# Kernel tuning notes

Hardware: AMD Instinct MI355X
Metric: run time of the kernel (lower is better)

Reference implementation:

```python
import jax, jax.numpy as jnp
from jax import lax
import numpy as np

B, T, LAT, HID, OUT, NC = 1024, 128, 128, 256, 128, 2
HODE = 128          # ODEFunc hidden width (hard-coded 128 in source)
H = LAT // 2        # LSTM hidden = latent_dim / 2


def setup_inputs() -> dict:
    key = jax.random.key(0)
    ks = jax.random.split(key, 8)
    s = 0.05
    f32 = jnp.float32
    return {
        "initial_state": jax.random.normal(ks[0], (B, LAT), f32),
        "time_steps": jnp.linspace(0.0, 1.0, T, dtype=f32),
        "ode_w1": jax.random.normal(ks[1], (HODE, LAT), f32) * s,
        "ode_b1": jnp.zeros((HODE,), f32),
        "ode_w2": jax.random.normal(ks[2], (LAT, HODE), f32) * s,
        "ode_b2": jnp.zeros((LAT,), f32),
        "l2h_w": jax.random.normal(ks[3], (HID, LAT), f32) * s,
        "l2h_b": jnp.zeros((HID,), f32),
        "h2o_w": jax.random.normal(ks[4], (OUT, HID), f32) * s,
        "h2o_b": jnp.zeros((OUT,), f32),
        "lstm_wih": jax.random.normal(ks[5], (4 * H, LAT), f32) * s,
        "lstm_whh": jax.random.normal(ks[6], (4 * H, H), f32) * s,
        "lstm_bih": jnp.zeros((4 * H,), f32),
        "lstm_bhh": jnp.zeros((4 * H,), f32),
        "fc2_w": jax.random.normal(ks[7], (NC, H), f32) * s,
        "fc2_b": jnp.zeros((NC,), f32),
    }


def reference(initial_state, time_steps, ode_w1, ode_b1, ode_w2, ode_b2,
              l2h_w, l2h_b, h2o_w, h2o_b,
              lstm_wih, lstm_whh, lstm_bih, lstm_bhh, fc2_w, fc2_b):
    def ode_f(y):  # Linear-ELU-Linear, time-independent
        return jax.nn.elu(y @ ode_w1.T + ode_b1) @ ode_w2.T + ode_b2

    def rk4_step(y, dt):
        k1 = ode_f(y)
        k2 = ode_f(y + 0.5 * dt * k1)
        k3 = ode_f(y + 0.5 * dt * k2)
        k4 = ode_f(y + dt * k3)
        y_new = y + (dt / 6.0) * (k1 + 2.0 * k2 + 2.0 * k3 + k4)
        return y_new, y_new

    dts = time_steps[1:] - time_steps[:-1]
    _, ys = lax.scan(rk4_step, initial_state, dts)
    zs = jnp.concatenate([initial_state[None], ys], axis=0)  # [T, B, LAT] = odeint output

    # torch: cat((initial_state.unsqueeze(0), zs)).permute(1,0,2) -> [B, T+1, LAT]
    input_lstm = jnp.concatenate([initial_state[None], zs], axis=0).transpose(1, 0, 2)

    # nn.LSTM is seq-first, so it scans dim0 (=B) with dim1 (=T+1) as its batch.
    h0 = jnp.zeros((input_lstm.shape[1], H), input_lstm.dtype)
    c0 = jnp.zeros_like(h0)

    def cell(carry, x):
        h, c = carry
        gates = x @ lstm_wih.T + lstm_bih + h @ lstm_whh.T + lstm_bhh
        i, f, g, o = jnp.split(gates, 4, axis=-1)  # torch gate order i,f,g,o
        c = jax.nn.sigmoid(f) * c + jax.nn.sigmoid(i) * jnp.tanh(g)
        h = jax.nn.sigmoid(o) * jnp.tanh(c)
        return (h, c), h

    _, lstm_hs = lax.scan(cell, (h0, c0), input_lstm)  # [B, T+1, H]
    lstm_out = lstm_hs[:, -1, :] @ fc2_w.T + fc2_b      # [B, NC]

    hs = zs @ l2h_w.T + l2h_b   # [T, B, HID]
    xs = hs @ h2o_w.T + h2o_b   # [T, B, OUT]
    return xs, lstm_out
```

## Files before the change

### kernel.cpp

```cpp
#include <hip/hip_runtime.h>


typedef short s16x8 __attribute__((ext_vector_type(8)));
typedef float f32x4 __attribute__((ext_vector_type(4)));
typedef _Float16 f16x2 __attribute__((ext_vector_type(2)));
typedef _Float16 f16x8 __attribute__((ext_vector_type(8)));

#define MFMA16(a, b, c) __builtin_amdgcn_mfma_f32_16x16x32_bf16((a), (b), (c), 0, 0, 0)

__device__ __forceinline__ void lds_barrier() {
  asm volatile("s_waitcnt lgkmcnt(0)\n\ts_barrier" ::: "memory");
}

__device__ __forceinline__ unsigned short f2bf(float x) {
  union { float f; unsigned u; } v; v.f = x;
  return (unsigned short)((v.u + 0x7FFFu + ((v.u >> 16) & 1u)) >> 16);
}

__device__ __forceinline__ unsigned cvtpk(float lo, float hi) {
  unsigned r;
  asm("v_cvt_pk_bf16_f32 %0, %1, %2" : "=v"(r) : "v"(lo), "v"(hi));
  return r;
}

__device__ __forceinline__ int swz(int row, int col2) {
  return row * 256 + (col2 ^ ((row & 15) << 4));
}

__device__ __forceinline__ f16x8 cvt8(const float* p) {
  float4 a = *(const float4*)p, b = *(const float4*)(p + 4);
  return (f16x8){(_Float16)a.x, (_Float16)a.y, (_Float16)a.z, (_Float16)a.w,
                 (_Float16)b.x, (_Float16)b.y, (_Float16)b.z, (_Float16)b.w};
}

__global__ __launch_bounds__(256, 1) void ode_kernel(
    const float* __restrict__ init, const float* __restrict__ ts,
    const float* __restrict__ w1, const float* __restrict__ b1,
    const float* __restrict__ w2, const float* __restrict__ b2,
    const float* __restrict__ wih, const float* __restrict__ bih,
    const float* __restrict__ bhh,
    unsigned short* __restrict__ zbuf, float* __restrict__ XW4)
{
  __shared__ __align__(16) unsigned char sY[4096];
  __shared__ __align__(16) unsigned char sH[4096];
  __shared__ __align__(16) float sYf[2048];
  const int tid = (int)threadIdx.x;
  const int w = tid >> 6, lane = tid & 63;
  const int l15 = lane & 15, l4 = lane >> 4;
  const int rowbase = (int)blockIdx.x * 16;
  const int colbase = w * 32;

  s16x8 w1f[2][4], w2f[2][4];
#pragma unroll
  for (int tc = 0; tc < 2; ++tc) {
    const int rj = colbase + 16 * tc + l15;
#pragma unroll
    for (int ks = 0; ks < 4; ++ks) {
      const int kb = ks * 32 + l4 * 8;
      s16x8 va, vb;
#pragma unroll
      for (int t = 0; t < 8; ++t) {
        va[t] = (short)f2bf(w1[rj * 128 + kb + t]);
        vb[t] = (short)f2bf(w2[rj * 128 + kb + t]);
      }
      w1f[tc][ks] = va; w2f[tc][ks] = vb;
    }
  }
  float b1v[2], b2v[2];
#pragma unroll
  for (int tc = 0; tc < 2; ++tc) {
    const int cc = colbase + 16 * tc + l15;
    b1v[tc] = b1[cc]; b2v[tc] = b2[cc];
  }

  int aOff[4];
#pragma unroll
  for (int ks = 0; ks < 4; ++ks) aOff[ks] = swz(l15, (ks * 32 + l4 * 8) * 2);
  int cOff[2][4];
#pragma unroll
  for (int tc = 0; tc < 2; ++tc)
#pragma unroll
    for (int r = 0; r < 4; ++r)
      cOff[tc][r] = swz(l4 * 4 + r, (colbase + 16 * tc + l15) * 2);

  float y0[2][4], yac[2][4];
#pragma unroll
  for (int tc = 0; tc < 2; ++tc)
#pragma unroll
    for (int r = 0; r < 4; ++r)
      y0[tc][r] = init[(rowbase + l4 * 4 + r) * 128 + colbase + 16 * tc + l15];

  {
    const int i = tid * 8;
    const int row = i >> 7, col = i & 127;
    union { unsigned short u[8]; s16x8 v; } p;
#pragma unroll
    for (int t = 0; t < 8; ++t) p.u[t] = f2bf(init[(rowbase + row) * 128 + col + t]);
    *(s16x8*)(sY + swz(row, col * 2)) = p.v;
    *(s16x8*)(zbuf + rowbase * 128 + i) = p.v;
  }
  __syncthreads();

  const f32x4 fz = {0.f, 0.f, 0.f, 0.f};

  for (int s = 0; s < 127; ++s) {
    const float dt = ts[s + 1] - ts[s];
    const float c16 = dt * (1.f / 6.f), c13 = dt * (1.f / 3.f), ch = dt * 0.5f;
#pragma unroll
    for (int st = 0; st < 4; ++st) {
      f32x4 acc[2];
      acc[0] = fz; acc[1] = fz;
#pragma unroll
      for (int ks = 0; ks < 4; ++ks) {
        s16x8 a = *(const s16x8*)(sY + aOff[ks]);
        acc[0] = MFMA16(a, w1f[0][ks], acc[0]);
        acc[1] = MFMA16(a, w1f[1][ks], acc[1]);
      }
#pragma unroll
      for (int r = 0; r < 4; ++r) {
        float v0 = acc[0][r] + b1v[0];
        float v1 = acc[1][r] + b1v[1];
        v0 = v0 > 0.f ? v0 : (__expf(v0) - 1.f);
        v1 = v1 > 0.f ? v1 : (__expf(v1) - 1.f);
        const unsigned p = cvtpk(v0, v1);
        *(unsigned short*)(sH + cOff[0][r]) = (unsigned short)p;
        *(unsigned short*)(sH + cOff[1][r]) = (unsigned short)(p >> 16);
      }
      lds_barrier();
      f32x4 kc[2];
      kc[0] = fz; kc[1] = fz;
#pragma unroll
      for (int ks = 0; ks < 4; ++ks) {
        s16x8 a = *(const s16x8*)(sH + aOff[ks]);
        kc[0] = MFMA16(a, w2f[0][ks], kc[0]);
        kc[1] = MFMA16(a, w2f[1][ks], kc[1]);
      }
#pragma unroll
      for (int r = 0; r < 4; ++r) {
        float yn2[2];
#pragma unroll
        for (int tc = 0; tc < 2; ++tc) {
          const float kv = kc[tc][r] + b2v[tc];
          float yn;
          if (st == 0)      { yac[tc][r] = fmaf(c16, kv, y0[tc][r]);  yn = fmaf(ch, kv, y0[tc][r]); }
          else if (st == 1) { yac[tc][r] = fmaf(c13, kv, yac[tc][r]); yn = fmaf(ch, kv, y0[tc][r]); }
          else if (st == 2) { yac[tc][r] = fmaf(c13, kv, yac[tc][r]); yn = fmaf(dt, kv, y0[tc][r]); }
          else              { y0[tc][r]  = fmaf(c16, kv, yac[tc][r]); yn = y0[tc][r]; }
          yn2[tc] = yn;
        }
        const unsigned p = cvtpk(yn2[0], yn2[1]);
        *(unsigned short*)(sY + cOff[0][r]) = (unsigned short)p;
        *(unsigned short*)(sY + cOff[1][r]) = (unsigned short)(p >> 16);
      }
      lds_barrier();
    }
    {
      const int i = tid * 8;
      const int row = i >> 7;
      const s16x8 v = *(const s16x8*)(sY + swz(row, (i & 127) * 2));
      *(s16x8*)(zbuf + (long)(s + 1) * 131072 + rowbase * 128 + i) = v;
    }
  }
#pragma unroll
  for (int tc = 0; tc < 2; ++tc)
#pragma unroll
    for (int r = 0; r < 4; ++r)
      sYf[(l4 * 4 + r) * 128 + colbase + 16 * tc + l15] = y0[tc][r];
  lds_barrier();
  {
    const int g = tid;
    const int q = g >> 6, j = g & 63;
#pragma unroll 4
    for (int tl = 0; tl < 16; ++tl) {
      float a0 = 0.f, a1 = 0.f, a2 = 0.f, a3 = 0.f;
#pragma unroll 8
      for (int k = 0; k < 32; ++k) {
        float4 wv = *(const float4*)(wih + g * 128 + 4 * k);
        float4 yv = *(const float4*)(sYf + tl * 128 + 4 * k);
        a0 = fmaf(wv.x, yv.x, a0); a1 = fmaf(wv.y, yv.y, a1);
        a2 = fmaf(wv.z, yv.z, a2); a3 = fmaf(wv.w, yv.w, a3);
      }
      XW4[(rowbase + tl) * 256 + j * 4 + q] = bih[g] + bhh[g] + ((a0 + a1) + (a2 + a3));
    }
  }
}

__global__ __launch_bounds__(128) void wf_kernel(
    const float* __restrict__ h2o, const float* __restrict__ l2h,
    const float* __restrict__ l2hb, const float* __restrict__ h2ob,
    unsigned short* __restrict__ wfo, float* __restrict__ bfo)
{
  const int o = (int)blockIdx.x, k = (int)threadIdx.x;
  float acc = 0.f;
  for (int h = 0; h < 256; ++h) acc = fmaf(h2o[o * 256 + h], l2h[h * 128 + k], acc);
  wfo[o * 128 + k] = f2bf(acc);
  __shared__ float red[128];
  red[k] = h2o[o * 256 + k] * l2hb[k] + h2o[o * 256 + 128 + k] * l2hb[128 + k];
  __syncthreads();
  for (int s = 64; s > 0; s >>= 1) {
    if (k < s) red[k] += red[k + s];
    __syncthreads();
  }
  if (k == 0) bfo[o] = red[0] + h2ob[o];
}

__device__ __forceinline__ void proj_body(
    const unsigned short* __restrict__ zbuf, const unsigned short* __restrict__ wf,
    const float* __restrict__ bfv_, float* __restrict__ xs)
{
  const int tid = (int)threadIdx.x;
  const int w = tid >> 6, lane = tid & 63;
  const int l15 = lane & 15, l4 = lane >> 4;
  const int colbase = w * 32;
  const long rowbase = (long)(blockIdx.x - 1) * 64;

  s16x8 wff[2][4];
#pragma unroll
  for (int tc = 0; tc < 2; ++tc) {
    const int rj = colbase + 16 * tc + l15;
#pragma unroll
    for (int ks = 0; ks < 4; ++ks)
      wff[tc][ks] = *(const s16x8*)(wf + rj * 128 + ks * 32 + l4 * 8);
  }
  const float bv0 = bfv_[colbase + l15], bv1 = bfv_[colbase + 16 + l15];

  const f32x4 fz = {0.f, 0.f, 0.f, 0.f};
  f32x4 acc[4][2];
#pragma unroll
  for (int rt = 0; rt < 4; ++rt) { acc[rt][0] = fz; acc[rt][1] = fz; }

#pragma unroll
  for (int rt = 0; rt < 4; ++rt) {
    const long rb = rowbase + rt * 16 + l15;
#pragma unroll
    for (int ks = 0; ks < 4; ++ks) {
      const s16x8 a = *(const s16x8*)(zbuf + rb * 128 + ks * 32 + l4 * 8);
      acc[rt][0] = MFMA16(a, wff[0][ks], acc[rt][0]);
      acc[rt][1] = MFMA16(a, wff[1][ks], acc[rt][1]);
    }
  }
#pragma unroll
  for (int rt = 0; rt < 4; ++rt)
#pragma unroll
    for (int r = 0; r < 4; ++r) {
      const long row = rowbase + rt * 16 + l4 * 4 + r;
      xs[row * 128 + colbase + l15]      = acc[rt][0][r] + bv0;
      xs[row * 128 + colbase + 16 + l15] = acc[rt][1][r] + bv1;
    }
}

__device__ __forceinline__ void lstm_body(
    const float* __restrict__ XW4,
    const float* __restrict__ whh,
    float* __restrict__ hsT)
{
  const int tid = (int)threadIdx.x;
  const int L = tid & 63;
  const int q = L & 3;
  const int j = (tid >> 6) * 16 + (L >> 2);
  const int row = q * 64 + j;

  __shared__ __align__(16) _Float16 hbuf[2][64];

  f16x8 wq[8];
#pragma unroll
  for (int k = 0; k < 8; ++k) wq[k] = cvt8(whh + row * 64 + 8 * k);

  const float Aa = (q == 2) ? 2.f : 1.f;
  const float Sa = (q == 2) ? -2.f : -1.f;
  const float Ba = (q == 2) ? -1.f : 0.f;

  if (tid < 64) hbuf[0][tid] = (_Float16)0.f;
  float c = 0.f;

  const int xwi = j * 4 + q;
  float xq[4];
#pragma unroll
  for (int i = 0; i < 4; ++i) xq[i] = XW4[i * 256 + xwi];
  lds_barrier();

  for (int tb = 0; tb < 256; ++tb) {
#pragma unroll
    for (int i = 0; i < 4; ++i) {
      const int t = tb * 4 + i;
      const int cur = i & 1;
      const float xw = xq[i];
      xq[i] = XW4[((t + 4) & 1023) * 256 + xwi];

      const f16x8* hb8 = (const f16x8*)hbuf[cur];
      float4 ac0 = {0.f, 0.f, 0.f, 0.f}, ac1 = {0.f, 0.f, 0.f, 0.f};
#pragma unroll
      for (int r = 0; r < 8; ++r) {
        const f16x8 v = hb8[r];
        float4& ac = (r & 1) ? ac1 : ac0;
        ac.x = __builtin_amdgcn_fdot2(__builtin_shufflevector(wq[r], wq[r], 0, 1),
                                      __builtin_shufflevector(v, v, 0, 1), ac.x, false);
        ac.y = __builtin_amdgcn_fdot2(__builtin_shufflevector(wq[r], wq[r], 2, 3),
                                      __builtin_shufflevector(v, v, 2, 3), ac.y, false);
        ac.z = __builtin_amdgcn_fdot2(__builtin_shufflevector(wq[r], wq[r], 4, 5),
                                      __builtin_shufflevector(v, v, 4, 5), ac.z, false);
        ac.w = __builtin_amdgcn_fdot2(__builtin_shufflevector(wq[r], wq[r], 6, 7),
                                      __builtin_shufflevector(v, v, 6, 7), ac.w, false);
      }
      const float pre = xw + (((ac0.x + ac0.y) + (ac0.z + ac0.w)) +
                              ((ac1.x + ac1.y) + (ac1.z + ac1.w)));
      const float act = fmaf(Aa, __builtin_amdgcn_rcpf(1.f + __expf(Sa * pre)), Ba);

      const int ai = __float_as_int(act);
      const float x1 = __int_as_float(__builtin_amdgcn_mov_dpp(ai, 0xB1, 0xF, 0xF, true));
      const float x2 = __int_as_float(__builtin_amdgcn_mov_dpp(ai, 0x4E, 0xF, 0xF, true));
      const float x3 = __int_as_float(__builtin_amdgcn_mov_dpp(ai, 0x1B, 0xF, 0xF, true));
      const float gi = (q == 0) ? act : (q == 1) ? x1 : (q == 2) ? x2 : x3;
      const float gf = (q == 0) ? x1 : (q == 1) ? act : (q == 2) ? x3 : x2;
      const float gg = (q == 0) ? x2 : (q == 1) ? x3 : (q == 2) ? act : x1;
      const float go = (q == 0) ? x3 : (q == 1) ? x2 : (q == 2) ? x1 : act;

      c = fmaf(gf, c, gi * gg);
      const float th = fmaf(2.f, __builtin_amdgcn_rcpf(1.f + __expf(-2.f * c)), -1.f);
      const float h = go * th;

      if (q == 0) {
        hbuf[cur ^ 1][j] = (_Float16)h;
        hsT[j * 1024 + t] = h;
      }
      lds_barrier();
    }
  }
}

__global__ __launch_bounds__(256, 1) void proj_lstm_kernel(
    const unsigned short* __restrict__ zbuf, const unsigned short* __restrict__ wf,
    const float* __restrict__ bfv_, float* __restrict__ xs,
    const float* __restrict__ XW4, const float* __restrict__ whh,
    float* __restrict__ hsT)
{
  if (blockIdx.x == 0) lstm_body(XW4, whh, hsT);
  else                 proj_body(zbuf, wf, bfv_, xs);
}

__global__ __launch_bounds__(256) void fc2_kernel(
    const float* __restrict__ hsT, const float* __restrict__ fw,
    const float* __restrict__ fb, float* __restrict__ lout)
{
  const int idx = (int)blockIdx.x * 256 + (int)threadIdx.x;
  const int n = idx >> 10, t = idx & 1023;
  float acc = fb[n];
#pragma unroll 8
  for (int j = 0; j < 64; ++j) acc = fmaf(fw[n * 64 + j], hsT[j * 1024 + t], acc);
  lout[t * 2 + n] = acc;
}

extern "C" void kernel_launch(void* const* d_in, const int* in_sizes, int n_in,
                              void* d_out, int out_size, void* d_ws, size_t ws_size,
                              hipStream_t stream) {
  const float* init  = (const float*)d_in[0];
  const float* ts    = (const float*)d_in[1];
  const float* ode_w1 = (const float*)d_in[2];
  const float* ode_b1 = (const float*)d_in[3];
  const float* ode_w2 = (const float*)d_in[4];
  const float* ode_b2 = (const float*)d_in[5];
  const float* l2h_w = (const float*)d_in[6];
  const float* l2h_b = (const float*)d_in[7];
  const float* h2o_w = (const float*)d_in[8];
  const float* h2o_b = (const float*)d_in[9];
  const float* wih   = (const float*)d_in[10];
  const float* whh   = (const float*)d_in[11];
  const float* bih   = (const float*)d_in[12];
  const float* bhh   = (const float*)d_in[13];
  const float* fc2w  = (const float*)d_in[14];
  const float* fc2b  = (const float*)d_in[15];

  char* ws = (char*)d_ws;
  unsigned short* zbuf  = (unsigned short*)(ws);
  float* XW4            = (float*)(ws + 33554432);
  float* hsT            = (float*)(ws + 34603008);
  unsigned short* wfbuf = (unsigned short*)(ws + 34865152);
  float* bfused         = (float*)(ws + 34897920);

  float* xs   = (float*)d_out;
  float* lout = xs + 16777216;

  ode_kernel<<<64, 256, 0, stream>>>(init, ts, ode_w1, ode_b1, ode_w2, ode_b2,
                                     wih, bih, bhh, zbuf, XW4);
  wf_kernel<<<128, 128, 0, stream>>>(h2o_w, l2h_w, l2h_b, h2o_b, wfbuf, bfused);
  proj_lstm_kernel<<<2049, 256, 0, stream>>>(zbuf, wfbuf, bfused, xs, XW4, whh, hsT);
  fc2_kernel<<<8, 256, 0, stream>>>(hsT, fc2w, fc2b, lout);
}
```

Measured before the change: 706.2 us.

## Process two 16-row groups per ODE block to interleave independent MFMA chains

Each ODE block now integrates 32 batch rows as two independent 16-row groups, with double LDS buffers, and the grid is halved from 64 to 32 blocks. The two groups' MFMAs are interleaved and each K-reduction is split into two partial chains that are summed afterwards. This is meant to hide MFMA dependency latency in the serial 127-step RK4 loop. The time-step value is also prefetched one step ahead. The cost is fewer blocks (less parallelism across CUs), more registers, and twice the per-block work in the final XW4 projection.

```diff
diff --git a/kernel.cpp b/kernel.cpp
--- a/kernel.cpp
+++ b/kernel.cpp
@@ -41,13 +41,13 @@
     const float* __restrict__ bhh,
     unsigned short* __restrict__ zbuf, float* __restrict__ XW4)
 {
-  __shared__ __align__(16) unsigned char sY[4096];
-  __shared__ __align__(16) unsigned char sH[4096];
-  __shared__ __align__(16) float sYf[2048];
+  __shared__ __align__(16) unsigned char sY[2][4096];
+  __shared__ __align__(16) unsigned char sH[2][4096];
+  __shared__ __align__(16) float sYf[4096];
   const int tid = (int)threadIdx.x;
   const int w = tid >> 6, lane = tid & 63;
   const int l15 = lane & 15, l4 = lane >> 4;
-  const int rowbase = (int)blockIdx.x * 16;
+  const int rowbase = (int)blockIdx.x * 32;
   const int colbase = w * 32;
 
   s16x8 w1f[2][4], w2f[2][4];
@@ -83,104 +83,148 @@
     for (int r = 0; r < 4; ++r)
       cOff[tc][r] = swz(l4 * 4 + r, (colbase + 16 * tc + l15) * 2);
 
-  float y0[2][4], yac[2][4];
-#pragma unroll
-  for (int tc = 0; tc < 2; ++tc)
-#pragma unroll
-    for (int r = 0; r < 4; ++r)
-      y0[tc][r] = init[(rowbase + l4 * 4 + r) * 128 + colbase + 16 * tc + l15];
+  float y0[2][2][4], yac[2][2][4];
+#pragma unroll
+  for (int g = 0; g < 2; ++g)
+#pragma unroll
+    for (int tc = 0; tc < 2; ++tc)
+#pragma unroll
+      for (int r = 0; r < 4; ++r)
+        y0[g][tc][r] = init[(rowbase + g * 16 + l4 * 4 + r) * 128 + colbase + 16 * tc + l15];
 
   {
     const int i = tid * 8;
     const int row = i >> 7, col = i & 127;
-    union { unsigned short u[8]; s16x8 v; } p;
-#pragma unroll
-    for (int t = 0; t < 8; ++t) p.u[t] = f2bf(init[(rowbase + row) * 128 + col + t]);
-    *(s16x8*)(sY + swz(row, col * 2)) = p.v;
-    *(s16x8*)(zbuf + rowbase * 128 + i) = p.v;
+#pragma unroll
+    for (int g = 0; g < 2; ++g) {
+      union { unsigned short u[8]; s16x8 v; } p;
+#pragma unroll
+      for (int t = 0; t < 8; ++t)
+        p.u[t] = f2bf(init[(rowbase + g * 16 + row) * 128 + col + t]);
+      *(s16x8*)(sY[g] + swz(row, col * 2)) = p.v;
+      *(s16x8*)(zbuf + (rowbase + g * 16) * 128 + i) = p.v;
+    }
   }
   __syncthreads();
 
   const f32x4 fz = {0.f, 0.f, 0.f, 0.f};
+  float t_cur = ts[0], t_next = ts[1];
 
   for (int s = 0; s < 127; ++s) {
-    const float dt = ts[s + 1] - ts[s];
+    const float t_next2 = (s < 126) ? ts[s + 2] : 0.f;
+    const float dt = t_next - t_cur;
     const float c16 = dt * (1.f / 6.f), c13 = dt * (1.f / 3.f), ch = dt * 0.5f;
 #pragma unroll
     for (int st = 0; st < 4; ++st) {
-      f32x4 acc[2];
-      acc[0] = fz; acc[1] = fz;
+      s16x8 aA[4], aB[4];
 #pragma unroll
       for (int ks = 0; ks < 4; ++ks) {
-        s16x8 a = *(const s16x8*)(sY + aOff[ks]);
-        acc[0] = MFMA16(a, w1f[0][ks], acc[0]);
-        acc[1] = MFMA16(a, w1f[1][ks], acc[1]);
-      }
-#pragma unroll
-      for (int r = 0; r < 4; ++r) {
-        float v0 = acc[0][r] + b1v[0];
-        float v1 = acc[1][r] + b1v[1];
-        v0 = v0 > 0.f ? v0 : (__expf(v0) - 1.f);
-        v1 = v1 > 0.f ? v1 : (__expf(v1) - 1.f);
-        const unsigned p = cvtpk(v0, v1);
-        *(unsigned short*)(sH + cOff[0][r]) = (unsigned short)p;
-        *(unsigned short*)(sH + cOff[1][r]) = (unsigned short)(p >> 16);
+        aA[ks] = *(const s16x8*)(sY[0] + aOff[ks]);
+        aB[ks] = *(const s16x8*)(sY[1] + aOff[ks]);
+      }
+      f32x4 accA[2], accB[2];
+      {
+        const f32x4 pA0 = MFMA16(aA[1], w1f[0][1], MFMA16(aA[0], w1f[0][0], fz));
+        const f32x4 qA0 = MFMA16(aB[1], w1f[0][1], MFMA16(aB[0], w1f[0][0], fz));
+        const f32x4 pA1 = MFMA16(aA[1], w1f[1][1], MFMA16(aA[0], w1f[1][0], fz));
+        const f32x4 qA1 = MFMA16(aB[1], w1f[1][1], MFMA16(aB[0], w1f[1][0], fz));
+        const f32x4 pB0 = MFMA16(aA[3], w1f[0][3], MFMA16(aA[2], w1f[0][2], fz));
+        const f32x4 qB0 = MFMA16(aB[3], w1f[0][3], MFMA16(aB[2], w1f[0][2], fz));
+        const f32x4 pB1 = MFMA16(aA[3], w1f[1][3], MFMA16(aA[2], w1f[1][2], fz));
+        const f32x4 qB1 = MFMA16(aB[3], w1f[1][3], MFMA16(aB[2], w1f[1][2], fz));
+        accA[0] = pA0 + pB0; accA[1] = pA1 + pB1;
+        accB[0] = qA0 + qB0; accB[1] = qA1 + qB1;
+      }
+#pragma unroll
+      for (int g = 0; g < 2; ++g) {
+        const f32x4* ac = (g == 0) ? accA : accB;
+#pragma unroll
+        for (int r = 0; r < 4; ++r) {
+          float v0 = ac[0][r] + b1v[0];
+          float v1 = ac[1][r] + b1v[1];
+          v0 = v0 > 0.f ? v0 : (__expf(v0) - 1.f);
+          v1 = v1 > 0.f ? v1 : (__expf(v1) - 1.f);
+          const unsigned p = cvtpk(v0, v1);
+          *(unsigned short*)(sH[g] + cOff[0][r]) = (unsigned short)p;
+          *(unsigned short*)(sH[g] + cOff[1][r]) = (unsigned short)(p >> 16);
+        }
       }
       lds_barrier();
-      f32x4 kc[2];
-      kc[0] = fz; kc[1] = fz;
+      s16x8 hA[4], hB[4];
 #pragma unroll
       for (int ks = 0; ks < 4; ++ks) {
-        s16x8 a = *(const s16x8*)(sH + aOff[ks]);
-        kc[0] = MFMA16(a, w2f[0][ks], kc[0]);
-        kc[1] = MFMA16(a, w2f[1][ks], kc[1]);
-      }
-#pragma unroll
-      for (int r = 0; r < 4; ++r) {
-        float yn2[2];
-#pragma unroll
-        for (int tc = 0; tc < 2; ++tc) {
-          const float kv = kc[tc][r] + b2v[tc];
-          float yn;
-          if (st == 0)      { yac[tc][r] = fmaf(c16, kv, y0[tc][r]);  yn = fmaf(ch, kv, y0[tc][r]); }
-          else if (st == 1) { yac[tc][r] = fmaf(c13, kv, yac[tc][r]); yn = fmaf(ch, kv, y0[tc][r]); }
-          else if (st == 2) { yac[tc][r] = fmaf(c13, kv, yac[tc][r]); yn = fmaf(dt, kv, y0[tc][r]); }
-          else              { y0[tc][r]  = fmaf(c16, kv, yac[tc][r]); yn = y0[tc][r]; }
-          yn2[tc] = yn;
+        hA[ks] = *(const s16x8*)(sH[0] + aOff[ks]);
+        hB[ks] = *(const s16x8*)(sH[1] + aOff[ks]);
+      }
+      f32x4 kcA[2], kcB[2];
+      {
+        const f32x4 pA0 = MFMA16(hA[1], w2f[0][1], MFMA16(hA[0], w2f[0][0], fz));
+        const f32x4 qA0 = MFMA16(hB[1], w2f[0][1], MFMA16(hB[0], w2f[0][0], fz));
+        const f32x4 pA1 = MFMA16(hA[1], w2f[1][1], MFMA16(hA[0], w2f[1][0], fz));
+        const f32x4 qA1 = MFMA16(hB[1], w2f[1][1], MFMA16(hB[0], w2f[1][0], fz));
+        const f32x4 pB0 = MFMA16(hA[3], w2f[0][3], MFMA16(hA[2], w2f[0][2], fz));
+        const f32x4 qB0 = MFMA16(hB[3], w2f[0][3], MFMA16(hB[2], w2f[0][2], fz));
+        const f32x4 pB1 = MFMA16(hA[3], w2f[1][3], MFMA16(hA[2], w2f[1][2], fz));
+        const f32x4 qB1 = MFMA16(hB[3], w2f[1][3], MFMA16(hB[2], w2f[1][2], fz));
+        kcA[0] = pA0 + pB0; kcA[1] = pA1 + pB1;
+        kcB[0] = qA0 + qB0; kcB[1] = qA1 + qB1;
+      }
+#pragma unroll
+      for (int g = 0; g < 2; ++g) {
+        const f32x4* kc = (g == 0) ? kcA : kcB;
+#pragma unroll
+        for (int r = 0; r < 4; ++r) {
+          float yn2[2];
+#pragma unroll
+          for (int tc = 0; tc < 2; ++tc) {
+            const float kv = kc[tc][r] + b2v[tc];
+            float yn;
+            if (st == 0)      { yac[g][tc][r] = fmaf(c16, kv, y0[g][tc][r]);  yn = fmaf(ch, kv, y0[g][tc][r]); }
+            else if (st == 1) { yac[g][tc][r] = fmaf(c13, kv, yac[g][tc][r]); yn = fmaf(ch, kv, y0[g][tc][r]); }
+            else if (st == 2) { yac[g][tc][r] = fmaf(c13, kv, yac[g][tc][r]); yn = fmaf(dt, kv, y0[g][tc][r]); }
+            else              { y0[g][tc][r]  = fmaf(c16, kv, yac[g][tc][r]); yn = y0[g][tc][r]; }
+            yn2[tc] = yn;
+          }
+          const unsigned p = cvtpk(yn2[0], yn2[1]);
+          *(unsigned short*)(sY[g] + cOff[0][r]) = (unsigned short)p;
+          *(unsigned short*)(sY[g] + cOff[1][r]) = (unsigned short)(p >> 16);
         }
-        const unsigned p = cvtpk(yn2[0], yn2[1]);
-        *(unsigned short*)(sY + cOff[0][r]) = (unsigned short)p;
-        *(unsigned short*)(sY + cOff[1][r]) = (unsigned short)(p >> 16);
       }
       lds_barrier();
     }
     {
       const int i = tid * 8;
       const int row = i >> 7;
-      const s16x8 v = *(const s16x8*)(sY + swz(row, (i & 127) * 2));
-      *(s16x8*)(zbuf + (long)(s + 1) * 131072 + rowbase * 128 + i) = v;
-    }
-  }
-#pragma unroll
-  for (int tc = 0; tc < 2; ++tc)
-#pragma unroll
-    for (int r = 0; r < 4; ++r)
-      sYf[(l4 * 4 + r) * 128 + colbase + 16 * tc + l15] = y0[tc][r];
+#pragma unroll
+      for (int g = 0; g < 2; ++g) {
+        const s16x8 v = *(const s16x8*)(sY[g] + swz(row, (i & 127) * 2));
+        *(s16x8*)(zbuf + (long)(s + 1) * 131072 + (rowbase + g * 16) * 128 + i) = v;
+      }
+    }
+    t_cur = t_next; t_next = t_next2;
+  }
+#pragma unroll
+  for (int g = 0; g < 2; ++g)
+#pragma unroll
+    for (int tc = 0; tc < 2; ++tc)
+#pragma unroll
+      for (int r = 0; r < 4; ++r)
+        sYf[(g * 16 + l4 * 4 + r) * 128 + colbase + 16 * tc + l15] = y0[g][tc][r];
   lds_barrier();
   {
-    const int g = tid;
-    const int q = g >> 6, j = g & 63;
+    const int gr = tid;
+    const int q = gr >> 6, j = gr & 63;
 #pragma unroll 4
-    for (int tl = 0; tl < 16; ++tl) {
+    for (int tl = 0; tl < 32; ++tl) {
       float a0 = 0.f, a1 = 0.f, a2 = 0.f, a3 = 0.f;
 #pragma unroll 8
       for (int k = 0; k < 32; ++k) {
-        float4 wv = *(const float4*)(wih + g * 128 + 4 * k);
+        float4 wv = *(const float4*)(wih + gr * 128 + 4 * k);
         float4 yv = *(const float4*)(sYf + tl * 128 + 4 * k);
         a0 = fmaf(wv.x, yv.x, a0); a1 = fmaf(wv.y, yv.y, a1);
         a2 = fmaf(wv.z, yv.z, a2); a3 = fmaf(wv.w, yv.w, a3);
       }
-      XW4[(rowbase + tl) * 256 + j * 4 + q] = bih[g] + bhh[g] + ((a0 + a1) + (a2 + a3));
+      XW4[(rowbase + tl) * 256 + j * 4 + q] = bih[gr] + bhh[gr] + ((a0 + a1) + (a2 + a3));
     }
   }
 }
@@ -380,7 +424,7 @@
   float* xs   = (float*)d_out;
   float* lout = xs + 16777216;
 
-  ode_kernel<<<64, 256, 0, stream>>>(init, ts, ode_w1, ode_b1, ode_w2, ode_b2,
+  ode_kernel<<<32, 256, 0, stream>>>(init, ts, ode_w1, ode_b1, ode_w2, ode_b2,
                                      wih, bih, bhh, zbuf, XW4);
   wf_kernel<<<128, 128, 0, stream>>>(h2o_w, l2h_w, l2h_b, h2o_b, wfbuf, bfused);
   proj_lstm_kernel<<<2049, 256, 0, stream>>>(zbuf, wfbuf, bfused, xs, XW4, whh, hsT);
```

Result: slower. 982.2 us (+39.1%).
